# Performance work log

Hardware: AMD Instinct MI355X
Metric: run time of the kernel (lower is better)

Reference implementation:

```python
import jax, jax.numpy as jnp
import numpy as np

N_NODES = 10000
N_EDGES = 160000
F_IN, D, DEPTH, F_OUT = 6, 512, 10, 1


def setup_inputs() -> dict:
    key = jax.random.key(0)
    ks = jax.random.split(key, 10)
    features = jax.random.normal(ks[0], (N_NODES, F_IN), dtype=jnp.float32)
    src = jax.random.randint(ks[1], (N_EDGES,), 0, N_NODES, dtype=jnp.int32)
    dst = jax.random.randint(ks[2], (N_EDGES,), 0, N_NODES, dtype=jnp.int32)
    s_in = 1.0 / np.sqrt(F_IN)
    s_h = 1.0 / np.sqrt(D)
    W_in = jax.random.uniform(ks[3], (F_IN, D), jnp.float32, -s_in, s_in)
    b_in = jax.random.uniform(ks[4], (D,), jnp.float32, -s_in, s_in)
    Ws = jax.random.uniform(ks[5], (DEPTH, D, D), jnp.float32, -s_h, s_h)
    bs = jax.random.uniform(ks[6], (DEPTH, D), jnp.float32, -s_h, s_h)
    W_out = jax.random.uniform(ks[7], (D, F_OUT), jnp.float32, -s_h, s_h)
    b_out = jax.random.uniform(ks[8], (F_OUT,), jnp.float32, -s_h, s_h)
    return {"features": features, "W_in": W_in, "b_in": b_in, "Ws": Ws,
            "bs": bs, "W_out": W_out, "b_out": b_out, "src": src, "dst": dst}


def reference(features, W_in, b_in, Ws, bs, W_out, b_out, src, dst):
    n = features.shape[0]
    # GCNLayer: aggregate = scatter-sum of neighbor features (copy_src + sum), then Linear
    agg = jax.ops.segment_sum(features[src], dst, num_segments=n)  # [N, F_in]
    x = jax.nn.relu(agg @ W_in + b_in)  # ReLU only after input layer (per forward)

    def step(x, wb):
        W, b = wb
        a = jax.ops.segment_sum(x[src], dst, num_segments=n)  # [N, D]
        return a @ W + b, None  # no activation between hidden GCN layers

    x, _ = jax.lax.scan(step, x, (Ws, bs))
    return x @ W_out + b_out  # [N, 1]
```

## Files before the change

### kernel.cpp

```cpp
#include <hip/hip_runtime.h>


#define N_NODES 10000
#define N_EDGES 160000
#define DEPTH   10

#define NB_G 40
#define NB_C 33
#define NB   (NB_G + NB_C)
#define BT   1024
#define NTHG (NB_G * BT)
#define NPB  250
#define ECAP 8192

typedef unsigned long long u64;

__device__ __forceinline__ int ldAi(const int* p) {
    return __hip_atomic_load(p, __ATOMIC_RELAXED, __HIP_MEMORY_SCOPE_AGENT);
}
__device__ __forceinline__ void stAi(int* p, int v) {
    __hip_atomic_store(p, v, __ATOMIC_RELAXED, __HIP_MEMORY_SCOPE_AGENT);
}
__device__ __forceinline__ float ldAf(const float* p) {
    return __hip_atomic_load(p, __ATOMIC_RELAXED, __HIP_MEMORY_SCOPE_AGENT);
}
__device__ __forceinline__ void stAf(float* p, float v) {
    __hip_atomic_store(p, v, __ATOMIC_RELAXED, __HIP_MEMORY_SCOPE_AGENT);
}
__device__ __forceinline__ u64 ld8(const u64* p) {
    return __hip_atomic_load(p, __ATOMIC_RELAXED, __HIP_MEMORY_SCOPE_AGENT);
}
__device__ __forceinline__ void st8(u64* p, u64 v) {
    __hip_atomic_store(p, v, __ATOMIC_RELAXED, __HIP_MEMORY_SCOPE_AGENT);
}
__device__ __forceinline__ u64 packf(float f) {
    union { float f; unsigned u; } c; c.f = f;
    return (1ull << 32) | (u64)c.u;
}
__device__ __forceinline__ float unpackf(u64 v) {
    union { unsigned u; float f; } c; c.u = (unsigned)v;
    return c.f;
}
#define READY(v) ((unsigned)((v) >> 32) != 0u)

__device__ __forceinline__ float pollf(const u64* p) {
    u64 v = ld8(p);
    while (!READY(v)) { __builtin_amdgcn_s_sleep(1); v = ld8(p); }
    return unpackf(v);
}

__device__ __forceinline__ void group_bar(int* flags, int gi, int n, int target) {
    const int tx = threadIdx.x;
    asm volatile("s_waitcnt vmcnt(0)" ::: "memory");
    __syncthreads();
    if (tx == 0) stAi(&flags[gi * 32], target);
    if (tx < n && tx != gi) {
        while (ldAi(&flags[tx * 32]) < target) __builtin_amdgcn_s_sleep(1);
    }
    __syncthreads();
}

extern "C" __global__ void __launch_bounds__(BT, 1) gcn_mega(
    const float* __restrict__ features, const float* __restrict__ W_in,
    const float* __restrict__ b_in, const float* __restrict__ Ws,
    const float* __restrict__ bs, const float* __restrict__ W_out,
    const float* __restrict__ b_out, const int* __restrict__ src,
    const int* __restrict__ dst, float* __restrict__ out,
    int* g_arrive, u64* gamma8, u64* vslab, int* deg, int* esrc,
    float* rb0, float* rb1, int* row_ptr, int* cursor)
{
    __shared__ int   lds_e[ECAP];
    __shared__ float s_Wb[4096];
    __shared__ float s_vt[512];
    __shared__ float s_gam[16];
    __shared__ int   s_info[2];
    __shared__ int   s_wsum[16];

    const int tx = threadIdx.x;
    const int bx = blockIdx.x;

    if (bx >= NB_G) {
        const int gi   = bx - NB_G;
        const int cw   = gi * 16 + (tx >> 6);
        const int lane = tx & 63;
        if (cw > 512) return;
        for (int s = 0; s < DEPTH; s++) {
            const int l = 9 - s;
            const float* rowp = (cw < 512)
                ? (Ws + (size_t)l * (512 * 512) + (size_t)cw * 512)
                : (bs + (size_t)l * 512);
            float wrow[8];
#pragma unroll
            for (int c = 0; c < 8; c++) wrow[c] = rowp[lane + 64 * c];
            float vin[8];
            if (s == 0) {
#pragma unroll
                for (int c = 0; c < 8; c++) vin[c] = W_out[lane + 64 * c];
            } else {
                const u64* vb = vslab + (size_t)s * 512;
                u64 raw[8];
#pragma unroll
                for (int c = 0; c < 8; c++) raw[c] = ld8(vb + lane + 64 * c);
                for (;;) {
                    bool ok = true;
#pragma unroll
                    for (int c = 0; c < 8; c++)
                        if (!READY(raw[c])) { ok = false; raw[c] = ld8(vb + lane + 64 * c); }
                    if (ok) break;
                    __builtin_amdgcn_s_sleep(1);
                }
#pragma unroll
                for (int c = 0; c < 8; c++) vin[c] = unpackf(raw[c]);
            }
            float acc = 0.f;
#pragma unroll
            for (int c = 0; c < 8; c++) acc += wrow[c] * vin[c];
#pragma unroll
            for (int off = 32; off; off >>= 1) acc += __shfl_xor(acc, off, 64);
            if (lane == 0) {
                if (cw < 512) st8(vslab + (size_t)(s + 1) * 512 + cw, packf(acc));
                else          st8(gamma8 + l, packf(acc));
            }
        }
        return;
    }

    const int gi = bx;
    int gt = 1;

    {
        const int t0 = bx * BT + tx;
        for (int e = t0; e < N_EDGES; e += NTHG) atomicAdd(&deg[dst[e]], 1);
    }
    for (int idx = tx; idx < 4096; idx += BT) {
        int j = idx >> 3, k = idx & 7;
        float v = 0.f;
        if (k < 6) v = W_in[k * 512 + j];
        else if (k == 6) v = b_in[j];
        s_Wb[idx] = v;
    }
    group_bar(g_arrive, gi, NB_G, gt++);

    if (bx == 0) {
        const int lane = tx & 63, wid = tx >> 6;
        const bool sact = tx < 1000;
        int lv[10];
        int ssum = 0;
        if (sact) {
#pragma unroll
            for (int i = 0; i < 10; i++) { lv[i] = ldAi(&deg[tx * 10 + i]); ssum += lv[i]; }
        }
        int v = ssum;
#pragma unroll
        for (int off = 1; off < 64; off <<= 1) {
            int u = __shfl_up(v, off, 64);
            if (lane >= off) v += u;
        }
        if (lane == 63) s_wsum[wid] = v;
        __syncthreads();
        if (wid == 0) {
            int w = (lane < 16) ? s_wsum[lane] : 0;
#pragma unroll
            for (int off = 1; off < 16; off <<= 1) {
                int u = __shfl_up(w, off, 64);
                if (lane >= off) w += u;
            }
            if (lane < 16) s_wsum[lane] = w;
        }
        __syncthreads();
        if (sact) {
            int run = (wid ? s_wsum[wid - 1] : 0) + (v - ssum);
#pragma unroll
            for (int i = 0; i < 10; i++) {
                stAi(&row_ptr[tx * 10 + i], run);
                stAi(&cursor[tx * 10 + i], run);
                run += lv[i];
            }
            if (tx == 999) stAi(&row_ptr[N_NODES], run);
        }
    }
    group_bar(g_arrive, gi, NB_G, gt++);

    {
        const int t0 = bx * BT + tx;
        for (int e = t0; e < N_EDGES; e += NTHG) {
            int d = dst[e];
            int sv = src[e];
            int pos = atomicAdd(&cursor[d], 1);
            stAi(&esrc[pos], sv);
        }
    }
    group_bar(g_arrive, gi, NB_G, gt++);

    if (tx == 0) {
        s_info[0] = ldAi(&row_ptr[bx * NPB]);
        s_info[1] = ldAi(&row_ptr[bx * NPB + NPB]);
    }
    __syncthreads();
    const int e_lo = s_info[0];
    const int slen = s_info[1] - e_lo;
    const bool use_lds = (slen <= ECAP);
    if (use_lds) {
        for (int i = tx; i < slen; i += BT) lds_e[i] = ldAi(&esrc[e_lo + i]);
    }
    __syncthreads();

    const int node = bx * NPB + (tx >> 2);
    const int sub  = tx & 3;
    const bool act = tx < 4 * NPB;
    int ns = 0, ne = 0;
    float a0 = 0.f, a1 = 0.f, a2 = 0.f, a3 = 0.f, a4 = 0.f, a5 = 0.f;
    if (act) {
        ns = ldAi(&row_ptr[node]);
        ne = ldAi(&row_ptr[node + 1]);
        for (int pp = ns + sub; pp < ne; pp += 4) {
            int j;
            if (use_lds) j = lds_e[pp - e_lo];
            else         j = ldAi(&esrc[pp]);
            const float2* f = (const float2*)(features + (size_t)j * 6);
            float2 f0 = f[0], f1 = f[1], f2 = f[2];
            a0 += f0.x; a1 += f0.y; a2 += f1.x;
            a3 += f1.y; a4 += f2.x; a5 += f2.y;
        }
        a0 += __shfl_xor(a0, 1, 64); a0 += __shfl_xor(a0, 2, 64);
        a1 += __shfl_xor(a1, 1, 64); a1 += __shfl_xor(a1, 2, 64);
        a2 += __shfl_xor(a2, 1, 64); a2 += __shfl_xor(a2, 2, 64);
        a3 += __shfl_xor(a3, 1, 64); a3 += __shfl_xor(a3, 2, 64);
        a4 += __shfl_xor(a4, 1, 64); a4 += __shfl_xor(a4, 2, 64);
        a5 += __shfl_xor(a5, 1, 64); a5 += __shfl_xor(a5, 2, 64);
    }

    if (tx < 512) s_vt[tx] = pollf(vslab + 10 * 512 + tx);
    else if (tx < 512 + DEPTH) s_gam[tx - 512] = pollf(gamma8 + (tx - 512));
    __syncthreads();

    if (act) {
        const float4* Wb4 = (const float4*)s_Wb;
        float zacc = 0.f;
#pragma unroll 4
        for (int jj = 0; jj < 128; jj++) {
            int j = (jj << 2) | sub;
            float4 wA = Wb4[2 * j];
            float4 wB = Wb4[2 * j + 1];
            float tv = wB.z + a0 * wA.x + a1 * wA.y + a2 * wA.z +
                       a3 * wA.w + a4 * wB.x + a5 * wB.y;
            zacc += fmaxf(tv, 0.f) * s_vt[j];
        }
        zacc += __shfl_xor(zacc, 1, 64);
        zacc += __shfl_xor(zacc, 2, 64);
        if (sub == 0) stAf(&rb0[node], zacc);
    }
    group_bar(g_arrive, gi, NB_G, gt++);

    for (int l = 0; l < DEPTH; l++) {
        if (act) {
            const float* rin = (l & 1) ? rb1 : rb0;
            float h0 = 0.f, h1 = 0.f, h2 = 0.f, h3 = 0.f;
            int pp = ns + sub;
            if (use_lds) {
                for (; pp + 12 < ne; pp += 16) {
                    h0 += ldAf(&rin[lds_e[pp - e_lo]]);
                    h1 += ldAf(&rin[lds_e[pp + 4 - e_lo]]);
                    h2 += ldAf(&rin[lds_e[pp + 8 - e_lo]]);
                    h3 += ldAf(&rin[lds_e[pp + 12 - e_lo]]);
                }
                for (; pp < ne; pp += 4) h0 += ldAf(&rin[lds_e[pp - e_lo]]);
            } else {
                for (; pp < ne; pp += 4) h0 += ldAf(&rin[ldAi(&esrc[pp])]);
            }
            float hs = (h0 + h1) + (h2 + h3);
            hs += __shfl_xor(hs, 1, 64);
            hs += __shfl_xor(hs, 2, 64);
            if (sub == 0) {
                float res = hs + s_gam[l];
                if (l == DEPTH - 1) out[node] = res + b_out[0];
                else stAf(&((l & 1) ? rb0 : rb1)[node], res);
            }
        }
        if (l < DEPTH - 1) group_bar(g_arrive, gi, NB_G, gt++);
    }
}


extern "C" void kernel_launch(void* const* d_in, const int* in_sizes, int n_in,
                              void* d_out, int out_size, void* d_ws, size_t ws_size,
                              hipStream_t stream) {
    const float* features = (const float*)d_in[0];
    const float* W_in     = (const float*)d_in[1];
    const float* b_in     = (const float*)d_in[2];
    const float* Ws       = (const float*)d_in[3];
    const float* bs       = (const float*)d_in[4];
    const float* W_out    = (const float*)d_in[5];
    const float* b_out    = (const float*)d_in[6];
    const int*   src      = (const int*)d_in[7];
    const int*   dst      = (const int*)d_in[8];
    float* out = (float*)d_out;

    char* base = (char*)d_ws;
    int*   g_arrive = (int*)(base + 0);
    u64*   gamma8   = (u64*)(base + 5120);
    u64*   vslab    = (u64*)(base + 5248);
    int*   deg      = (int*)(base + 50304);
    float* rb0      = (float*)(base + 90368);
    float* rb1      = (float*)(base + 130432);
    const size_t MEMSET_END = 170496;
    int* esrc       = (int*)(base + 170496);
    int* row_ptr    = (int*)(base + 810496);
    int* cursor     = (int*)(base + 850560);

    hipMemsetAsync(base, 0, MEMSET_END, stream);

    gcn_mega<<<NB, BT, 0, stream>>>(features, W_in, b_in, Ws, bs, W_out, b_out,
                                    src, dst, out,
                                    g_arrive, gamma8, vslab, deg, esrc,
                                    rb0, rb1, row_ptr, cursor);
}
```

Before: 205.1 us.

## Shrink weight-chain helper blocks to 5 with register-resident rows and group barriers

The helper blocks that fold the hidden weight matrices into a single vector (W_l · v chain) drop from 33 to 5. Each wavefront now holds 8 rows of a layer in registers, prefetching the next layer's rows while it waits. The per-element packed ready-flag polling is replaced by double-buffered plain float vectors, a group barrier across the 5 helper blocks, and a completion rendezvous flag the main blocks wait on. This cuts flag traffic and per-element spin loops, but each helper block now does more work per step and all helpers must synchronise every step.

After: 201.8 us. About the same (-1.6%).

```diff
diff --git a/kernel.cpp b/kernel.cpp
--- a/kernel.cpp
+++ b/kernel.cpp
@@ -6,7 +6,7 @@
 #define DEPTH   10
 
 #define NB_G 40
-#define NB_C 33
+#define NB_C 5
 #define NB   (NB_G + NB_C)
 #define BT   1024
 #define NTHG (NB_G * BT)
@@ -29,24 +29,6 @@
 }
 __device__ __forceinline__ u64 ld8(const u64* p) {
     return __hip_atomic_load(p, __ATOMIC_RELAXED, __HIP_MEMORY_SCOPE_AGENT);
-}
-__device__ __forceinline__ void st8(u64* p, u64 v) {
-    __hip_atomic_store(p, v, __ATOMIC_RELAXED, __HIP_MEMORY_SCOPE_AGENT);
-}
-__device__ __forceinline__ u64 packf(float f) {
-    union { float f; unsigned u; } c; c.f = f;
-    return (1ull << 32) | (u64)c.u;
-}
-__device__ __forceinline__ float unpackf(u64 v) {
-    union { unsigned u; float f; } c; c.u = (unsigned)v;
-    return c.f;
-}
-#define READY(v) ((unsigned)((v) >> 32) != 0u)
-
-__device__ __forceinline__ float pollf(const u64* p) {
-    u64 v = ld8(p);
-    while (!READY(v)) { __builtin_amdgcn_s_sleep(1); v = ld8(p); }
-    return unpackf(v);
 }
 
 __device__ __forceinline__ void group_bar(int* flags, int gi, int n, int target) {
@@ -66,8 +48,8 @@
     const float* __restrict__ bs, const float* __restrict__ W_out,
     const float* __restrict__ b_out, const int* __restrict__ src,
     const int* __restrict__ dst, float* __restrict__ out,
-    int* g_arrive, u64* gamma8, u64* vslab, int* deg, int* esrc,
-    float* rb0, float* rb1, int* row_ptr, int* cursor)
+    int* g_arrive, int* c_arrive, int* rdv, float* gamma_f, float* vbufs,
+    int* deg, int* esrc, float* rb0, float* rb1, int* row_ptr, int* cursor)
 {
     __shared__ int   lds_e[ECAP];
     __shared__ float s_Wb[4096];
@@ -80,48 +62,89 @@
     const int bx = blockIdx.x;
 
     if (bx >= NB_G) {
-        const int gi   = bx - NB_G;
-        const int cw   = gi * 16 + (tx >> 6);
+        const int ci   = bx - NB_G;
+        const int gw   = ci * 16 + (tx >> 6);
         const int lane = tx & 63;
-        if (cw > 512) return;
+        const bool rows_job  = (gw < 64);
+        const bool gamma_job = (gw == 64);
+        const int  R0 = gw * 8;
+
+        float w[8][8];
+        if (rows_job) {
+            const float* Wl = Ws + (size_t)9 * 512 * 512;
+#pragma unroll
+            for (int r = 0; r < 8; r++) {
+                const float4* p = (const float4*)(Wl + (size_t)(R0 + r) * 512 + lane * 8);
+                float4 x = p[0], y = p[1];
+                w[r][0] = x.x; w[r][1] = x.y; w[r][2] = x.z; w[r][3] = x.w;
+                w[r][4] = y.x; w[r][5] = y.y; w[r][6] = y.z; w[r][7] = y.w;
+            }
+        } else if (gamma_job) {
+            const float4* p = (const float4*)(bs + (size_t)9 * 512 + lane * 8);
+            float4 x = p[0], y = p[1];
+            w[0][0] = x.x; w[0][1] = x.y; w[0][2] = x.z; w[0][3] = x.w;
+            w[0][4] = y.x; w[0][5] = y.y; w[0][6] = y.z; w[0][7] = y.w;
+        }
+
         for (int s = 0; s < DEPTH; s++) {
-            const int l = 9 - s;
-            const float* rowp = (cw < 512)
-                ? (Ws + (size_t)l * (512 * 512) + (size_t)cw * 512)
-                : (bs + (size_t)l * 512);
-            float wrow[8];
-#pragma unroll
-            for (int c = 0; c < 8; c++) wrow[c] = rowp[lane + 64 * c];
+            if (s > 0) group_bar(c_arrive, ci, NB_C, s);
             float vin[8];
             if (s == 0) {
-#pragma unroll
-                for (int c = 0; c < 8; c++) vin[c] = W_out[lane + 64 * c];
+                const float4* p = (const float4*)(W_out + lane * 8);
+                float4 x = p[0], y = p[1];
+                vin[0] = x.x; vin[1] = x.y; vin[2] = x.z; vin[3] = x.w;
+                vin[4] = y.x; vin[5] = y.y; vin[6] = y.z; vin[7] = y.w;
             } else {
-                const u64* vb = vslab + (size_t)s * 512;
-                u64 raw[8];
-#pragma unroll
-                for (int c = 0; c < 8; c++) raw[c] = ld8(vb + lane + 64 * c);
-                for (;;) {
-                    bool ok = true;
-#pragma unroll
-                    for (int c = 0; c < 8; c++)
-                        if (!READY(raw[c])) { ok = false; raw[c] = ld8(vb + lane + 64 * c); }
-                    if (ok) break;
-                    __builtin_amdgcn_s_sleep(1);
+                const u64* vb = (const u64*)(vbufs + (s & 1) * 512);
+#pragma unroll
+                for (int k = 0; k < 4; k++) {
+                    union { u64 u; float f[2]; } c;
+                    c.u = ld8(vb + lane * 4 + k);
+                    vin[2 * k]     = c.f[0];
+                    vin[2 * k + 1] = c.f[1];
                 }
-#pragma unroll
-                for (int c = 0; c < 8; c++) vin[c] = unpackf(raw[c]);
-            }
-            float acc = 0.f;
-#pragma unroll
-            for (int c = 0; c < 8; c++) acc += wrow[c] * vin[c];
-#pragma unroll
-            for (int off = 32; off; off >>= 1) acc += __shfl_xor(acc, off, 64);
-            if (lane == 0) {
-                if (cw < 512) st8(vslab + (size_t)(s + 1) * 512 + cw, packf(acc));
-                else          st8(gamma8 + l, packf(acc));
-            }
-        }
+            }
+            if (rows_job) {
+                float* vout = vbufs + ((s + 1) & 1) * 512;
+#pragma unroll
+                for (int r = 0; r < 8; r++) {
+                    float acc = 0.f;
+#pragma unroll
+                    for (int k = 0; k < 8; k++) acc += w[r][k] * vin[k];
+#pragma unroll
+                    for (int off = 32; off; off >>= 1) acc += __shfl_xor(acc, off, 64);
+                    if (lane == r) stAf(&vout[R0 + r], acc);
+                }
+            } else if (gamma_job) {
+                float acc = 0.f;
+#pragma unroll
+                for (int k = 0; k < 8; k++) acc += w[0][k] * vin[k];
+#pragma unroll
+                for (int off = 32; off; off >>= 1) acc += __shfl_xor(acc, off, 64);
+                if (lane == 0) stAf(&gamma_f[9 - s], acc);
+            }
+            if (s < DEPTH - 1) {
+                const int ln = 8 - s;
+                if (rows_job) {
+                    const float* Wl = Ws + (size_t)ln * 512 * 512;
+#pragma unroll
+                    for (int r = 0; r < 8; r++) {
+                        const float4* p = (const float4*)(Wl + (size_t)(R0 + r) * 512 + lane * 8);
+                        float4 x = p[0], y = p[1];
+                        w[r][0] = x.x; w[r][1] = x.y; w[r][2] = x.z; w[r][3] = x.w;
+                        w[r][4] = y.x; w[r][5] = y.y; w[r][6] = y.z; w[r][7] = y.w;
+                    }
+                } else if (gamma_job) {
+                    const float4* p = (const float4*)(bs + (size_t)ln * 512 + lane * 8);
+                    float4 x = p[0], y = p[1];
+                    w[0][0] = x.x; w[0][1] = x.y; w[0][2] = x.z; w[0][3] = x.w;
+                    w[0][4] = y.x; w[0][5] = y.y; w[0][6] = y.z; w[0][7] = y.w;
+                }
+            }
+        }
+        asm volatile("s_waitcnt vmcnt(0)" ::: "memory");
+        __syncthreads();
+        if (tx == 0) stAi(&rdv[ci * 32], 1);
         return;
     }
 
@@ -230,8 +253,12 @@
         a5 += __shfl_xor(a5, 1, 64); a5 += __shfl_xor(a5, 2, 64);
     }
 
-    if (tx < 512) s_vt[tx] = pollf(vslab + 10 * 512 + tx);
-    else if (tx < 512 + DEPTH) s_gam[tx - 512] = pollf(gamma8 + (tx - 512));
+    if (tx < NB_C) {
+        while (ldAi(&rdv[tx * 32]) < 1) __builtin_amdgcn_s_sleep(1);
+    }
+    __syncthreads();
+    if (tx < 512) s_vt[tx] = ldAf(&vbufs[tx]);
+    else if (tx < 512 + DEPTH) s_gam[tx - 512] = ldAf(&gamma_f[tx - 512]);
     __syncthreads();
 
     if (act) {
@@ -298,20 +325,22 @@
 
     char* base = (char*)d_ws;
     int*   g_arrive = (int*)(base + 0);
-    u64*   gamma8   = (u64*)(base + 5120);
-    u64*   vslab    = (u64*)(base + 5248);
-    int*   deg      = (int*)(base + 50304);
-    float* rb0      = (float*)(base + 90368);
-    float* rb1      = (float*)(base + 130432);
-    const size_t MEMSET_END = 170496;
-    int* esrc       = (int*)(base + 170496);
-    int* row_ptr    = (int*)(base + 810496);
-    int* cursor     = (int*)(base + 850560);
+    int*   c_arrive = (int*)(base + 5120);
+    int*   rdv      = (int*)(base + 5760);
+    float* gamma_f  = (float*)(base + 6400);
+    int*   deg      = (int*)(base + 6528);
+    float* rb0      = (float*)(base + 46592);
+    float* rb1      = (float*)(base + 86656);
+    const size_t MEMSET_END = 126720;
+    float* vbufs    = (float*)(base + 126720);
+    int*   esrc     = (int*)(base + 130816);
+    int*   row_ptr  = (int*)(base + 770816);
+    int*   cursor   = (int*)(base + 810880);
 
     hipMemsetAsync(base, 0, MEMSET_END, stream);
 
     gcn_mega<<<NB, BT, 0, stream>>>(features, W_in, b_in, Ws, bs, W_out, b_out,
                                     src, dst, out,
-                                    g_arrive, gamma8, vslab, deg, esrc,
-                                    rb0, rb1, row_ptr, cursor);
-}
+                                    g_arrive, c_arrive, rdv, gamma_f, vbufs,
+                                    deg, esrc, rb0, rb1, row_ptr, cursor);
+}
```
